# Performance work log

Hardware: AMD Instinct MI355X
Metric: run time of the kernel (lower is better)

The kernel has to match this reference:

```python
import jax, jax.numpy as jnp
import numpy as np

IN_FEAT, H_FEAT, NUM_CLASSES = 7, 8, 2
N_NODES, N_EDGES, N_GRAPHS = 40000, 640000, 64
DIMS = [IN_FEAT, H_FEAT, H_FEAT * 2, H_FEAT * 4, H_FEAT * 8, H_FEAT * 16]  # 7,8,16,32,64,128


def setup_inputs() -> dict:
    key = jax.random.key(0)
    ks = jax.random.split(key, 20)
    inp = {
        "x": jax.random.normal(ks[0], (N_NODES, IN_FEAT), dtype=jnp.float32),
        "edge_index": jax.random.randint(ks[1], (2, N_EDGES), 0, N_NODES, dtype=jnp.int32),
        "edge_attr": jax.random.uniform(ks[2], (N_EDGES,), dtype=jnp.float32),
        "batch": jnp.sort(jax.random.randint(ks[3], (N_NODES,), 0, N_GRAPHS, dtype=jnp.int32)),
    }
    # GraphConv params: lin_rel (with bias) applied to aggregated messages,
    # lin_root (no bias) applied to x itself. Stored as [in, out]; y = x @ W.
    for i in range(5):
        fi, fo = DIMS[i], DIMS[i + 1]
        s = 1.0 / np.sqrt(fi)
        inp[f"w_rel{i+1}"] = jax.random.uniform(ks[4 + 3 * i], (fi, fo), minval=-s, maxval=s, dtype=jnp.float32)
        inp[f"b_rel{i+1}"] = jax.random.uniform(ks[5 + 3 * i], (fo,), minval=-s, maxval=s, dtype=jnp.float32)
        inp[f"w_root{i+1}"] = jax.random.uniform(ks[6 + 3 * i], (fi, fo), minval=-s, maxval=s, dtype=jnp.float32)
    s = 1.0 / np.sqrt(DIMS[-1])
    inp["w_lin"] = jax.random.uniform(ks[19], (DIMS[-1], NUM_CLASSES), minval=-s, maxval=s, dtype=jnp.float32)
    inp["b_lin"] = jax.random.uniform(jax.random.fold_in(key, 99), (NUM_CLASSES,), minval=-s, maxval=s, dtype=jnp.float32)
    return inp


def graph_conv(x, src, dst, ew, w_rel, b_rel, w_root):
    # message: edge_weight * x[src]; aggregate by sum at dst (PyG GraphConv, aggr='add')
    msg = x[src] * ew[:, None]                               # [E, Fin]
    agg = jax.ops.segment_sum(msg, dst, num_segments=N_NODES)  # [N, Fin]
    return agg @ w_rel + b_rel + x @ w_root                  # [N, Fout]


def reference(x, edge_index, edge_attr, batch,
              w_rel1, b_rel1, w_root1, w_rel2, b_rel2, w_root2,
              w_rel3, b_rel3, w_root3, w_rel4, b_rel4, w_root4,
              w_rel5, b_rel5, w_root5, w_lin, b_lin):
    src, dst = edge_index[0], edge_index[1]
    h = x
    params = [(w_rel1, b_rel1, w_root1), (w_rel2, b_rel2, w_root2),
              (w_rel3, b_rel3, w_root3), (w_rel4, b_rel4, w_root4),
              (w_rel5, b_rel5, w_root5)]
    for wr, br, wo in params:
        h = graph_conv(h, src, dst, edge_attr, wr, br, wo)
    pooled = jax.ops.segment_sum(h, batch, num_segments=N_GRAPHS)  # [G, 128]
    return pooled @ w_lin + b_lin                                  # [G, 2]
```

## Files before the change

kernel.cpp:

```cpp
#include <hip/hip_runtime.h>

#define N_NODES 40000
#define N_EDGES 640000
#define N_GRAPHS 64
#define BCAP 64

typedef unsigned short u16;
typedef unsigned int u32;
typedef __attribute__((ext_vector_type(8))) short bf16x8;
typedef __attribute__((ext_vector_type(4))) float f32x4;

static inline int cdiv(long long a, int b) { return (int)((a + b - 1) / b); }

__device__ __forceinline__ u16 f2bf(float f) {
    u32 u = __float_as_uint(f);
    u32 r = (u + 0x7fffu + ((u >> 16) & 1u)) >> 16;
    return (u16)r;
}
__device__ __forceinline__ u32 packpair(float a, float b) {
    return (u32)f2bf(a) | ((u32)f2bf(b) << 16);
}
__device__ __forceinline__ void unpack8(uint4 q, float* o) {
    o[0] = __uint_as_float(q.x << 16); o[1] = __uint_as_float(q.x & 0xffff0000u);
    o[2] = __uint_as_float(q.y << 16); o[3] = __uint_as_float(q.y & 0xffff0000u);
    o[4] = __uint_as_float(q.z << 16); o[5] = __uint_as_float(q.z & 0xffff0000u);
    o[6] = __uint_as_float(q.w << 16); o[7] = __uint_as_float(q.w & 0xffff0000u);
}

__device__ __forceinline__ void pack_one(int idx, int KS, int Kreal, int FOUT,
                                         const float* __restrict__ wrel,
                                         const float* __restrict__ wroot,
                                         u16* __restrict__ out) {
    int j = idx & 7;
    int lane = (idx >> 3) & 63;
    int rest = idx >> 9;
    int nt = rest / KS, ks = rest - nt * KS;
    int k = ks * 32 + (lane >> 4) * 8 + j;
    int col = nt * 16 + (lane & 15);
    float v = 0.f;
    if (k < Kreal / 2) v = wrel[k * FOUT + col];
    else if (k < Kreal) v = wroot[(k - Kreal / 2) * FOUT + col];
    out[idx] = f2bf(v);
}

__global__ __launch_bounds__(256) void prep_kernel(
        const float* __restrict__ x, u16* __restrict__ xbf,
        const float* __restrict__ wr2, const float* __restrict__ wo2,
        const float* __restrict__ wr3, const float* __restrict__ wo3,
        const float* __restrict__ wr4, const float* __restrict__ wo4,
        const float* __restrict__ wr5, const float* __restrict__ wo5,
        const float* __restrict__ br5, const float* __restrict__ w_lin,
        u16* __restrict__ p2, u16* __restrict__ p3, u16* __restrict__ p4,
        int* __restrict__ deg, float* __restrict__ Szero,
        float* __restrict__ M, float* __restrict__ bb) {
    int tid = blockIdx.x * 256 + threadIdx.x;
    if (tid < 40000) {
        int n = tid;
        float v[8];
        #pragma unroll
        for (int i = 0; i < 7; ++i) v[i] = x[n * 7 + i];
        v[7] = 0.f;
        uint4 q;
        q.x = packpair(v[0], v[1]); q.y = packpair(v[2], v[3]);
        q.z = packpair(v[4], v[5]); q.w = packpair(v[6], v[7]);
        *(uint4*)(xbf + (long long)n * 8) = q;
    } else if (tid < 45632) {
        int t = tid - 40000;
        if (t < 512)        pack_one(t,        1, 16, 16, wr2, wo2, p2);
        else if (t < 1536)  pack_one(t - 512,  1, 32, 32, wr3, wo3, p3);
        else                pack_one(t - 1536, 2, 64, 64, wr4, wo4, p4);
    } else if (tid < 85632) {
        deg[tid - 45632] = 0;
    } else if (tid < 93888) {
        Szero[tid - 85632] = 0.f;
    } else if (tid < 94144) {
        int t = tid - 93888;
        int k = t >> 1, c = t & 1;
        const float* wk = (k < 64) ? (wr5 + k * 128) : (wo5 + (k - 64) * 128);
        float a = 0.f;
        for (int j = 0; j < 128; ++j) a += wk[j] * w_lin[j * 2 + c];
        M[t] = a;
    } else if (tid < 94146) {
        int c = tid - 94144;
        float a = 0.f;
        for (int j = 0; j < 128; ++j) a += br5[j] * w_lin[j * 2 + c];
        bb[c] = a;
    }
}

__global__ __launch_bounds__(256) void scatter_bucket(const int* __restrict__ src,
                                                      const int* __restrict__ dst,
                                                      const float* __restrict__ ew,
                                                      int* __restrict__ deg,
                                                      int2* __restrict__ pair) {
    int e = blockIdx.x * 256 + threadIdx.x;
    if (e >= N_EDGES) return;
    int d = dst[e];
    int pos = atomicAdd(&deg[d], 1);
    if (pos < BCAP) {
        int2 q;
        q.x = src[e];
        q.y = __float_as_int(ew[e]);
        pair[(long long)d * BCAP + pos] = q;
    }
}

__global__ __launch_bounds__(256) void gather_node1(const u16* __restrict__ xbf,
                                                    const int* __restrict__ deg,
                                                    const int2* __restrict__ pair,
                                                    const float* __restrict__ wr,
                                                    const float* __restrict__ br,
                                                    const float* __restrict__ wo,
                                                    u16* __restrict__ h2) {
    __shared__ float swr[56], swo[56], sb[8];
    if (threadIdx.x < 56) { swr[threadIdx.x] = wr[threadIdx.x]; swo[threadIdx.x] = wo[threadIdx.x]; }
    if (threadIdx.x < 8) sb[threadIdx.x] = br[threadIdx.x];
    __syncthreads();
    int tid = blockIdx.x * 256 + threadIdx.x;
    int n = tid >> 3;
    if (n >= N_NODES) return;
    int s3 = tid & 7;
    int dn = deg[n]; if (dn > BCAP) dn = BCAP;
    const int2* row = pair + (long long)n * BCAP;
    float acc[8] = {0.f, 0.f, 0.f, 0.f, 0.f, 0.f, 0.f, 0.f};
    int p = s3;
    int s = 0; float w = 0.f;
    if (p < dn) { int2 q = row[p]; s = q.x; w = __int_as_float(q.y); }
    while (p < dn) {
        uint4 rq = *(const uint4*)(xbf + (long long)s * 8);
        float wc = w;
        int pn = p + 8;
        if (pn < dn) { int2 q = row[pn]; s = q.x; w = __int_as_float(q.y); }
        float tv[8];
        unpack8(rq, tv);
        #pragma unroll
        for (int j = 0; j < 8; ++j) acc[j] = fmaf(wc, tv[j], acc[j]);
        p = pn;
    }
    #pragma unroll
    for (int d = 1; d < 8; d <<= 1) {
        #pragma unroll
        for (int j = 0; j < 8; ++j) acc[j] += __shfl_xor(acc[j], d, 64);
    }
    uint4 qh = *(const uint4*)(xbf + (long long)n * 8);
    float h[8];
    unpack8(qh, h);
    float o = sb[s3];
    #pragma unroll
    for (int i = 0; i < 7; ++i)
        o = fmaf(acc[i], swr[i * 8 + s3], fmaf(h[i], swo[i * 8 + s3], o));
    h2[(long long)n * 8 + s3] = f2bf(o);
}

template<int LOGF, int SLOG>
__global__ __launch_bounds__(256) void gather_bf16(const u16* __restrict__ hin,
                                                   const int* __restrict__ deg,
                                                   const int2* __restrict__ pair,
                                                   u16* __restrict__ agg) {
    constexpr int FIN = 8 << LOGF;
    constexpr int S = 1 << SLOG;
    long long tid = (long long)blockIdx.x * 256 + threadIdx.x;
    int n = (int)(tid >> (LOGF + SLOG));
    if (n >= N_NODES) return;
    int sub = (int)(tid & ((1 << (LOGF + SLOG)) - 1));
    int c = sub & ((1 << LOGF) - 1);
    int half = sub >> LOGF;
    const u16* base = hin + c * 8;
    int dn = deg[n]; if (dn > BCAP) dn = BCAP;
    const int2* row = pair + (long long)n * BCAP;
    float acc[8] = {0.f, 0.f, 0.f, 0.f, 0.f, 0.f, 0.f, 0.f};
    int p = half;
    int s = 0; float w = 0.f;
    if (p < dn) { int2 q = row[p]; s = q.x; w = __int_as_float(q.y); }
    while (p < dn) {
        uint4 rq = *(const uint4*)(base + (long long)s * FIN);
        float wc = w;
        int pn = p + S;
        if (pn < dn) { int2 q = row[pn]; s = q.x; w = __int_as_float(q.y); }
        float tv[8];
        unpack8(rq, tv);
        #pragma unroll
        for (int j = 0; j < 8; ++j) acc[j] = fmaf(wc, tv[j], acc[j]);
        p = pn;
    }
    #pragma unroll
    for (int d = (1 << LOGF); d < (1 << (LOGF + SLOG)); d <<= 1) {
        #pragma unroll
        for (int j = 0; j < 8; ++j) acc[j] += __shfl_xor(acc[j], d, 64);
    }
    if (half == 0) {
        uint4 o;
        o.x = packpair(acc[0], acc[1]); o.y = packpair(acc[2], acc[3]);
        o.z = packpair(acc[4], acc[5]); o.w = packpair(acc[6], acc[7]);
        *(uint4*)(agg + (long long)n * FIN + c * 8) = o;
    }
}

template<int FIN, int FOUT>
__global__ __launch_bounds__(64) void node_mfma(const u16* __restrict__ agg,
                                                const u16* __restrict__ hin,
                                                const u16* __restrict__ bpack,
                                                const float* __restrict__ b_rel,
                                                u16* __restrict__ hout) {
    constexpr int KREAL = 2 * FIN;
    constexpr int K = (KREAL < 32) ? 32 : KREAL;
    constexpr int KS = K / 32;
    constexpr int NT = FOUT / 16;
    int lane = threadIdx.x;
    int tile = blockIdx.x;
    int col = lane & 15;
    int node_a = tile * 16 + col;
    int kgrp = (lane >> 4) * 8;

    f32x4 acc[NT];
    #pragma unroll
    for (int nt = 0; nt < NT; ++nt) {
        float bv = b_rel[nt * 16 + col];
        acc[nt] = (f32x4){bv, bv, bv, bv};
    }

    #pragma unroll
    for (int ks = 0; ks < KS; ++ks) {
        int k0 = ks * 32 + kgrp;
        bf16x8 af;
        if (k0 < FIN)
            af = *(const bf16x8*)(agg + (long long)node_a * FIN + k0);
        else if (k0 < KREAL)
            af = *(const bf16x8*)(hin + (long long)node_a * FIN + (k0 - FIN));
        else
            af = (bf16x8)(short)0;
        #pragma unroll
        for (int nt = 0; nt < NT; ++nt) {
            bf16x8 bf = *(const bf16x8*)(bpack + (((nt * KS + ks) << 6) + lane) * 8);
            acc[nt] = __builtin_amdgcn_mfma_f32_16x16x32_bf16(af, bf, acc[nt], 0, 0, 0);
        }
    }

    int row0 = tile * 16 + (lane >> 4) * 4;
    #pragma unroll
    for (int nt = 0; nt < NT; ++nt)
        #pragma unroll
        for (int r = 0; r < 4; ++r)
            hout[(long long)(row0 + r) * FOUT + nt * 16 + col] = f2bf(acc[nt][r]);
}

__global__ __launch_bounds__(256) void seg_pool(const u16* __restrict__ agg5,
                                                const u16* __restrict__ h5,
                                                const int* __restrict__ batch,
                                                float* __restrict__ S_rel,
                                                float* __restrict__ S_root,
                                                float* __restrict__ cnt) {
    int wv = threadIdx.x >> 6, lane = threadIdx.x & 63;
    int n0 = blockIdx.x * 40 + (wv & 1) * 20;
    int n1 = n0 + 20;
    if (n0 >= N_NODES) return;
    if (n1 > N_NODES) n1 = N_NODES;
    bool isRel = (wv < 2);
    const u16* buf = isRel ? agg5 : h5;
    float* Sout = isRel ? S_rel : S_root;
    bool doCnt = (!isRel) && (lane == 0);

    float acc = 0.f, c_acc = 0.f;
    int cur = batch[n0];
    for (int n = n0; n < n1; ++n) {
        int g = batch[n];
        float v = __uint_as_float((u32)buf[(long long)n * 64 + lane] << 16);
        if (g != cur) {
            atomicAdd(&Sout[cur * 64 + lane], acc);
            if (doCnt) atomicAdd(&cnt[cur], c_acc);
            acc = 0.f; c_acc = 0.f;
            cur = g;
        }
        acc += v;
        c_acc += 1.f;
    }
    atomicAdd(&Sout[cur * 64 + lane], acc);
    if (doCnt) atomicAdd(&cnt[cur], c_acc);
}

__global__ void final_kernel(const float* __restrict__ S_rel,
                             const float* __restrict__ S_root,
                             const float* __restrict__ cnt,
                             const float* __restrict__ M,
                             const float* __restrict__ bb,
                             const float* __restrict__ b_lin,
                             float* __restrict__ out) {
    int tid = threadIdx.x;
    int g = tid >> 1;
    int c = tid & 1;
    float acc = b_lin[c] + cnt[g] * bb[c];
    #pragma unroll 8
    for (int k = 0; k < 64; ++k) {
        acc += S_rel[g * 64 + k] * M[k * 2 + c];
        acc += S_root[g * 64 + k] * M[(64 + k) * 2 + c];
    }
    out[g * 2 + c] = acc;
}

extern "C" void kernel_launch(void* const* d_in, const int* in_sizes, int n_in,
                              void* d_out, int out_size, void* d_ws, size_t ws_size,
                              hipStream_t stream) {
    const float* x     = (const float*)d_in[0];
    const int*   ei    = (const int*)d_in[1];
    const float* ea    = (const float*)d_in[2];
    const int*   batch = (const int*)d_in[3];
    const int* src = ei;
    const int* dst = ei + N_EDGES;

    const float* w_rel[5], *b_rel[5], *w_root[5];
    for (int i = 0; i < 5; ++i) {
        w_rel[i]  = (const float*)d_in[4 + 3 * i];
        b_rel[i]  = (const float*)d_in[5 + 3 * i];
        w_root[i] = (const float*)d_in[6 + 3 * i];
    }
    const float* w_lin = (const float*)d_in[19];
    const float* b_lin = (const float*)d_in[20];
    float* out = (float*)d_out;

    u16*   xbf     = (u16*)d_ws;
    u16*   agg     = xbf + 320000;
    u16*   h2      = agg + 2560000;
    u16*   h3      = h2 + 320000;
    u16*   h4      = h3 + 640000;
    u16*   h5      = h4 + 1280000;
    u16*   p2      = h5 + 2560000;
    u16*   p3      = p2 + 512;
    u16*   p4      = p3 + 1024;
    float* S_rel   = (float*)(p4 + 4096);
    float* S_root  = S_rel + 4096;
    float* cnt     = S_root + 4096;
    float* M       = cnt + 64;
    float* bb      = M + 256;
    int2*  pair    = (int2*)(bb + 4);
    int*   deg     = (int*)(pair + (long long)N_NODES * BCAP);

    const int BLK = 256;
    const int EB = cdiv(N_EDGES, BLK);

    prep_kernel<<<368, BLK, 0, stream>>>(x, xbf,
                                         w_rel[1], w_root[1], w_rel[2], w_root[2],
                                         w_rel[3], w_root[3], w_rel[4], w_root[4],
                                         b_rel[4], w_lin,
                                         p2, p3, p4, deg, S_rel, M, bb);

    scatter_bucket<<<EB, BLK, 0, stream>>>(src, dst, ea, deg, pair);

    gather_node1<<<1250, BLK, 0, stream>>>(xbf, deg, pair, w_rel[0], b_rel[0], w_root[0], h2);

    gather_bf16<0, 3><<<cdiv((long long)N_NODES * 8, BLK), BLK, 0, stream>>>(
        h2, deg, pair, agg);
    node_mfma<8, 16><<<2500, 64, 0, stream>>>(agg, h2, p2, b_rel[1], h3);

    gather_bf16<1, 3><<<cdiv((long long)N_NODES * 16, BLK), BLK, 0, stream>>>(
        h3, deg, pair, agg);
    node_mfma<16, 32><<<2500, 64, 0, stream>>>(agg, h3, p3, b_rel[2], h4);

    gather_bf16<2, 3><<<cdiv((long long)N_NODES * 32, BLK), BLK, 0, stream>>>(
        h4, deg, pair, agg);
    node_mfma<32, 64><<<2500, 64, 0, stream>>>(agg, h4, p4, b_rel[3], h5);

    gather_bf16<3, 3><<<cdiv((long long)N_NODES * 64, BLK), BLK, 0, stream>>>(
        h5, deg, pair, agg);
    seg_pool<<<1000, BLK, 0, stream>>>(agg, h5, batch, S_rel, S_root, cnt);

    final_kernel<<<1, 128, 0, stream>>>(S_rel, S_root, cnt, M, bb, b_lin, out);
}
```

Before: 213.6 us.

## Batch gather loads for memory parallelism and fuse pooling into last layers

Replaces the serial software-pipelined gather loop with fully unrolled batched loads: all pair entries first, then all feature rows, then the FMAs. This raises memory-level parallelism. The root-side graph pooling moves into the last node_mfma epilogue via atomics, and the final aggregation is fused with rel-side pooling in a new gather_pool5 kernel. This removes the agg5 write/read and the separate seg_pool kernel. The cost is more registers per thread, which can lower occupancy, plus many more global atomics.

```diff
diff --git a/kernel.cpp b/kernel.cpp
--- a/kernel.cpp
+++ b/kernel.cpp
@@ -122,20 +122,29 @@
     int s3 = tid & 7;
     int dn = deg[n]; if (dn > BCAP) dn = BCAP;
     const int2* row = pair + (long long)n * BCAP;
+    int2 q[8];
+    #pragma unroll
+    for (int i = 0; i < 8; ++i) {
+        int p = s3 + i * 8;
+        if (p < dn) q[i] = row[p];
+    }
+    uint4 rq[8];
+    #pragma unroll
+    for (int i = 0; i < 8; ++i) {
+        int p = s3 + i * 8;
+        if (p < dn) rq[i] = *(const uint4*)(xbf + (long long)q[i].x * 8);
+    }
     float acc[8] = {0.f, 0.f, 0.f, 0.f, 0.f, 0.f, 0.f, 0.f};
-    int p = s3;
-    int s = 0; float w = 0.f;
-    if (p < dn) { int2 q = row[p]; s = q.x; w = __int_as_float(q.y); }
-    while (p < dn) {
-        uint4 rq = *(const uint4*)(xbf + (long long)s * 8);
-        float wc = w;
-        int pn = p + 8;
-        if (pn < dn) { int2 q = row[pn]; s = q.x; w = __int_as_float(q.y); }
-        float tv[8];
-        unpack8(rq, tv);
-        #pragma unroll
-        for (int j = 0; j < 8; ++j) acc[j] = fmaf(wc, tv[j], acc[j]);
-        p = pn;
+    #pragma unroll
+    for (int i = 0; i < 8; ++i) {
+        int p = s3 + i * 8;
+        if (p < dn) {
+            float tv[8];
+            unpack8(rq[i], tv);
+            float w = __int_as_float(q[i].y);
+            #pragma unroll
+            for (int j = 0; j < 8; ++j) acc[j] = fmaf(w, tv[j], acc[j]);
+        }
     }
     #pragma unroll
     for (int d = 1; d < 8; d <<= 1) {
@@ -159,6 +168,7 @@
                                                    u16* __restrict__ agg) {
     constexpr int FIN = 8 << LOGF;
     constexpr int S = 1 << SLOG;
+    constexpr int MAXIT = BCAP / S;
     long long tid = (long long)blockIdx.x * 256 + threadIdx.x;
     int n = (int)(tid >> (LOGF + SLOG));
     if (n >= N_NODES) return;
@@ -168,20 +178,30 @@
     const u16* base = hin + c * 8;
     int dn = deg[n]; if (dn > BCAP) dn = BCAP;
     const int2* row = pair + (long long)n * BCAP;
+
+    int2 q[MAXIT];
+    #pragma unroll
+    for (int i = 0; i < MAXIT; ++i) {
+        int p = half + i * S;
+        if (p < dn) q[i] = row[p];
+    }
+    uint4 rq[MAXIT];
+    #pragma unroll
+    for (int i = 0; i < MAXIT; ++i) {
+        int p = half + i * S;
+        if (p < dn) rq[i] = *(const uint4*)(base + (long long)q[i].x * FIN);
+    }
     float acc[8] = {0.f, 0.f, 0.f, 0.f, 0.f, 0.f, 0.f, 0.f};
-    int p = half;
-    int s = 0; float w = 0.f;
-    if (p < dn) { int2 q = row[p]; s = q.x; w = __int_as_float(q.y); }
-    while (p < dn) {
-        uint4 rq = *(const uint4*)(base + (long long)s * FIN);
-        float wc = w;
-        int pn = p + S;
-        if (pn < dn) { int2 q = row[pn]; s = q.x; w = __int_as_float(q.y); }
-        float tv[8];
-        unpack8(rq, tv);
-        #pragma unroll
-        for (int j = 0; j < 8; ++j) acc[j] = fmaf(wc, tv[j], acc[j]);
-        p = pn;
+    #pragma unroll
+    for (int i = 0; i < MAXIT; ++i) {
+        int p = half + i * S;
+        if (p < dn) {
+            float tv[8];
+            unpack8(rq[i], tv);
+            float w = __int_as_float(q[i].y);
+            #pragma unroll
+            for (int j = 0; j < 8; ++j) acc[j] = fmaf(w, tv[j], acc[j]);
+        }
     }
     #pragma unroll
     for (int d = (1 << LOGF); d < (1 << (LOGF + SLOG)); d <<= 1) {
@@ -196,12 +216,69 @@
     }
 }
 
-template<int FIN, int FOUT>
+__global__ __launch_bounds__(256) void gather_pool5(const u16* __restrict__ h5,
+                                                    const int* __restrict__ deg,
+                                                    const int2* __restrict__ pair,
+                                                    const int* __restrict__ batch,
+                                                    float* __restrict__ S_rel) {
+    long long tid = (long long)blockIdx.x * 256 + threadIdx.x;
+    int n = (int)(tid >> 6);
+    if (n >= N_NODES) return;
+    int lane = (int)(tid & 63);
+    int c = lane & 7;
+    int half = lane >> 3;
+    const u16* base = h5 + c * 8;
+    int dn = deg[n]; if (dn > BCAP) dn = BCAP;
+    const int2* row = pair + (long long)n * BCAP;
+
+    int2 q[8];
+    #pragma unroll
+    for (int i = 0; i < 8; ++i) {
+        int p = half + i * 8;
+        if (p < dn) q[i] = row[p];
+    }
+    uint4 rq[8];
+    #pragma unroll
+    for (int i = 0; i < 8; ++i) {
+        int p = half + i * 8;
+        if (p < dn) rq[i] = *(const uint4*)(base + (long long)q[i].x * 64);
+    }
+    float acc[8] = {0.f, 0.f, 0.f, 0.f, 0.f, 0.f, 0.f, 0.f};
+    #pragma unroll
+    for (int i = 0; i < 8; ++i) {
+        int p = half + i * 8;
+        if (p < dn) {
+            float tv[8];
+            unpack8(rq[i], tv);
+            float w = __int_as_float(q[i].y);
+            #pragma unroll
+            for (int j = 0; j < 8; ++j) acc[j] = fmaf(w, tv[j], acc[j]);
+        }
+    }
+    #pragma unroll
+    for (int d = 8; d < 64; d <<= 1) {
+        #pragma unroll
+        for (int j = 0; j < 8; ++j) acc[j] += __shfl_xor(acc[j], d, 64);
+    }
+    float val = 0.f;
+    #pragma unroll
+    for (int j = 0; j < 8; ++j) {
+        float t = __shfl(acc[j], lane >> 3, 64);
+        if ((lane & 7) == j) val = t;
+    }
+    int g = batch[n];
+    atomicAdd(&S_rel[g * 64 + lane], val);
+}
+
+template<int FIN, int FOUT, bool POOL>
 __global__ __launch_bounds__(64) void node_mfma(const u16* __restrict__ agg,
                                                 const u16* __restrict__ hin,
                                                 const u16* __restrict__ bpack,
                                                 const float* __restrict__ b_rel,
-                                                u16* __restrict__ hout) {
+                                                u16* __restrict__ hout,
+                                                const int* __restrict__ batch,
+                                                float* __restrict__ S_root,
+                                                float* __restrict__ cnt) {
     constexpr int KREAL = 2 * FIN;
     constexpr int K = (KREAL < 32) ? 32 : KREAL;
     constexpr int KS = K / 32;
@@ -242,40 +319,30 @@
         #pragma unroll
         for (int r = 0; r < 4; ++r)
             hout[(long long)(row0 + r) * FOUT + nt * 16 + col] = f2bf(acc[nt][r]);
-}
-
-__global__ __launch_bounds__(256) void seg_pool(const u16* __restrict__ agg5,
-                                                const u16* __restrict__ h5,
-                                                const int* __restrict__ batch,
-                                                float* __restrict__ S_rel,
-                                                float* __restrict__ S_root,
-                                                float* __restrict__ cnt) {
-    int wv = threadIdx.x >> 6, lane = threadIdx.x & 63;
-    int n0 = blockIdx.x * 40 + (wv & 1) * 20;
-    int n1 = n0 + 20;
-    if (n0 >= N_NODES) return;
-    if (n1 > N_NODES) n1 = N_NODES;
-    bool isRel = (wv < 2);
-    const u16* buf = isRel ? agg5 : h5;
-    float* Sout = isRel ? S_rel : S_root;
-    bool doCnt = (!isRel) && (lane == 0);
-
-    float acc = 0.f, c_acc = 0.f;
-    int cur = batch[n0];
-    for (int n = n0; n < n1; ++n) {
-        int g = batch[n];
-        float v = __uint_as_float((u32)buf[(long long)n * 64 + lane] << 16);
-        if (g != cur) {
-            atomicAdd(&Sout[cur * 64 + lane], acc);
-            if (doCnt) atomicAdd(&cnt[cur], c_acc);
-            acc = 0.f; c_acc = 0.f;
-            cur = g;
+
+    if constexpr (POOL) {
+        int b_first = batch[tile * 16];
+        int b_last = batch[tile * 16 + 15];
+        if (b_first == b_last) {
+            #pragma unroll
+            for (int nt = 0; nt < NT; ++nt) {
+                float s = acc[nt][0] + acc[nt][1] + acc[nt][2] + acc[nt][3];
+                s += __shfl_xor(s, 16, 64);
+                s += __shfl_xor(s, 32, 64);
+                if (lane < 16) atomicAdd(&S_root[b_first * FOUT + nt * 16 + col], s);
+            }
+            if (lane == 0) atomicAdd(&cnt[b_first], 16.f);
+        } else {
+            #pragma unroll
+            for (int r = 0; r < 4; ++r) {
+                int g = batch[row0 + r];
+                #pragma unroll
+                for (int nt = 0; nt < NT; ++nt)
+                    atomicAdd(&S_root[g * FOUT + nt * 16 + col], acc[nt][r]);
+                if (col == 0) atomicAdd(&cnt[g], 1.f);
+            }
         }
-        acc += v;
-        c_acc += 1.f;
-    }
-    atomicAdd(&Sout[cur * 64 + lane], acc);
-    if (doCnt) atomicAdd(&cnt[cur], c_acc);
+    }
 }
 
 __global__ void final_kernel(const float* __restrict__ S_rel,
@@ -319,7 +386,7 @@
 
     u16*   xbf     = (u16*)d_ws;
     u16*   agg     = xbf + 320000;
-    u16*   h2      = agg + 2560000;
+    u16*   h2      = agg + 1280000;
     u16*   h3      = h2 + 320000;
     u16*   h4      = h3 + 640000;
     u16*   h5      = h4 + 1280000;
@@ -349,19 +416,20 @@
 
     gather_bf16<0, 3><<<cdiv((long long)N_NODES * 8, BLK), BLK, 0, stream>>>(
         h2, deg, pair, agg);
-    node_mfma<8, 16><<<2500, 64, 0, stream>>>(agg, h2, p2, b_rel[1], h3);
+    node_mfma<8, 16, false><<<2500, 64, 0, stream>>>(agg, h2, p2, b_rel[1], h3,
+                                                     nullptr, nullptr, nullptr);
 
     gather_bf16<1, 3><<<cdiv((long long)N_NODES * 16, BLK), BLK, 0, stream>>>(
         h3, deg, pair, agg);
-    node_mfma<16, 32><<<2500, 64, 0, stream>>>(agg, h3, p3, b_rel[2], h4);
+    node_mfma<16, 32, false><<<2500, 64, 0, stream>>>(agg, h3, p3, b_rel[2], h4,
+                                                      nullptr, nullptr, nullptr);
 
     gather_bf16<2, 3><<<cdiv((long long)N_NODES * 32, BLK), BLK, 0, stream>>>(
         h4, deg, pair, agg);
-    node_mfma<32, 64><<<2500, 64, 0, stream>>>(agg, h4, p4, b_rel[3], h5);
-
-    gather_bf16<3, 3><<<cdiv((long long)N_NODES * 64, BLK), BLK, 0, stream>>>(
-        h5, deg, pair, agg);
-    seg_pool<<<1000, BLK, 0, stream>>>(agg, h5, batch, S_rel, S_root, cnt);
+    node_mfma<32, 64, true><<<2500, 64, 0, stream>>>(agg, h4, p4, b_rel[3], h5,
+                                                     batch, S_root, cnt);
+
+    gather_pool5<<<10000, BLK, 0, stream>>>(h5, deg, pair, batch, S_rel);
 
     final_kernel<<<1, 128, 0, stream>>>(S_rel, S_root, cnt, M, bb, b_lin, out);
 }
```

Result: slower. 257.4 us (+20.5%).
